# Optimization experiments

Hardware: AMD Instinct MI355X
Metric: run time of the kernel (lower is better)

The kernel has to match this reference:

```python
import jax, jax.numpy as jnp
import numpy as np
import math

LN_EPS = 1e-5


def setup_inputs() -> dict:
    key = jax.random.key(0)
    ks = jax.random.split(key, 6)
    B, S, D = 4, 4096, 1024
    x = jax.random.normal(ks[0], (B, S, D), dtype=jnp.float32)
    # torch.nn.Linear default init ~ U(-1/sqrt(fan_in), 1/sqrt(fan_in)); use scaled normal
    W_omega = jax.random.normal(ks[1], (D, D), dtype=jnp.float32) / math.sqrt(D)
    b_omega = jnp.zeros((D,), dtype=jnp.float32)
    log_scale = jnp.full((D,), math.log(0.1), dtype=jnp.float32)
    ln_gamma = jnp.ones((4 * D,), dtype=jnp.float32)
    ln_beta = jnp.zeros((4 * D,), dtype=jnp.float32)
    W1 = jax.random.normal(ks[2], (2 * D, 4 * D), dtype=jnp.float32) / math.sqrt(4 * D)
    b1 = jnp.zeros((2 * D,), dtype=jnp.float32)
    W2 = jax.random.normal(ks[3], (D, 2 * D), dtype=jnp.float32) / math.sqrt(2 * D)
    b2 = jnp.zeros((D,), dtype=jnp.float32)
    return {"x": x, "W_omega": W_omega, "b_omega": b_omega, "log_scale": log_scale,
            "ln_gamma": ln_gamma, "ln_beta": ln_beta, "W1": W1, "b1": b1, "W2": W2, "b2": b2}


def _layernorm(h, gamma, beta):
    mu = jnp.mean(h, axis=-1, keepdims=True)
    var = jnp.var(h, axis=-1, keepdims=True)
    return (h - mu) * jax.lax.rsqrt(var + LN_EPS) * gamma + beta


def reference(x, W_omega, b_omega, log_scale, ln_gamma, ln_beta, W1, b1, W2, b2):
    B, S, D = x.shape
    omega = jnp.einsum('bsd,ed->bse', x, W_omega) + b_omega  # Linear(dim, dim)
    position = jnp.arange(1, S + 1, dtype=x.dtype).reshape(1, S, 1)
    pos_scale = 1.0 / jnp.sqrt(position)
    omega_scaled = omega * jnp.exp(log_scale) * pos_scale
    phi = jnp.cumsum(omega_scaled, axis=1)
    cos_phi = jnp.cos(phi)
    sin_phi = jnp.sin(phi)
    cm_real = x * cos_phi  # content modulated (also cumsum input)
    cm_imag = x * sin_phi
    mem_real = jnp.cumsum(cm_real, axis=1) / position
    mem_imag = jnp.cumsum(cm_imag, axis=1) / position
    ret_real = mem_real * cos_phi + mem_imag * sin_phi
    ret_imag = mem_imag * cos_phi - mem_real * sin_phi
    context = jnp.concatenate([cm_real, cm_imag, ret_real, ret_imag], axis=-1)  # [B,S,4D]
    h = _layernorm(context, ln_gamma, ln_beta)
    h = jnp.einsum('bsd,ed->bse', h, W1) + b1
    h = jax.nn.gelu(h, approximate=False)  # torch nn.GELU default is exact erf form
    h = jnp.einsum('bsd,ed->bse', h, W2) + b2  # dropout is identity in eval mode
    return x + h
```

## Files before the change

kernel.cpp:

```cpp
#include <hip/hip_runtime.h>
#include <math.h>
#include <stddef.h>

#define BB 4
#define SS 4096
#define DD 1024

typedef unsigned short u16;
typedef __attribute__((ext_vector_type(4))) float f32x4;
typedef __attribute__((ext_vector_type(8))) short short8;
typedef __attribute__((ext_vector_type(4))) unsigned short u16x4;

#define EPI_BIAS  0
#define EPI_GELU  1
#define EPI_RESID 2

__device__ __forceinline__ u16 f2bf(float f) {
    unsigned u = __builtin_bit_cast(unsigned, f);
    u = (u + 0x7fffu + ((u >> 16) & 1u)) >> 16;
    return (u16)u;
}
__device__ __forceinline__ float bf2f(u16 h) {
    unsigned u = ((unsigned)h) << 16;
    return __builtin_bit_cast(float, u);
}

__device__ __forceinline__ void gll16(const void* g, void* l) {
    __builtin_amdgcn_global_load_lds(
        (const __attribute__((address_space(1))) void*)g,
        (__attribute__((address_space(3))) void*)l, 16, 0, 0);
}

template <int EPI>
__global__ __launch_bounds__(256) void gemm_bf(
    const u16* __restrict__ A, const u16* __restrict__ B,
    const float* __restrict__ bias, const float* __restrict__ resid,
    void* __restrict__ Cout, int M, int N, int K)
{
    __shared__ __align__(16) u16 Asm[128 * 64];
    __shared__ __align__(16) u16 Bsm[128 * 64];

    const int t = threadIdx.x;
    const int lane = t & 63;
    const int wave = t >> 6;
    const int wr = wave >> 1, wc = wave & 1;
    const int l15 = lane & 15, l4 = lane >> 4;
    const int bm = blockIdx.y * 128, bn = blockIdx.x * 128;

    const int r8 = lane >> 3, ch = lane & 7;
    const int schunk = ((ch ^ r8) << 3);

    const unsigned rmask = (unsigned)((l15 & 7) << 4);
    unsigned aoff[4][2], boff[4][2];
#pragma unroll
    for (int m = 0; m < 4; ++m)
#pragma unroll
        for (int ks = 0; ks < 2; ++ks) {
            const unsigned kb = ((((unsigned)ks << 6) | ((unsigned)l4 << 4)) ^ rmask);
            aoff[m][ks] = (unsigned)((wr * 64 + m * 16 + l15) * 128) + kb;
            boff[m][ks] = (unsigned)((wc * 64 + m * 16 + l15) * 128) + kb;
        }

    f32x4 acc[4][4];
#pragma unroll
    for (int m = 0; m < 4; ++m)
#pragma unroll
        for (int n = 0; n < 4; ++n) acc[m][n] = (f32x4)0.f;

    const char* acb = (const char*)Asm;
    const char* bcb = (const char*)Bsm;

    for (int k0 = 0; k0 < K; k0 += 64) {
        __syncthreads();
#pragma unroll
        for (int j = 0; j < 4; ++j) {
            const int rr = (wave * 4 + j) * 8 + r8;
            gll16(A + (size_t)(bm + rr) * K + k0 + schunk, (void*)(Asm + (wave * 4 + j) * 512));
            gll16(B + (size_t)(bn + rr) * K + k0 + schunk, (void*)(Bsm + (wave * 4 + j) * 512));
        }
        __syncthreads();
#pragma unroll
        for (int ks = 0; ks < 2; ++ks) {
            short8 af[4], bfr[4];
#pragma unroll
            for (int m = 0; m < 4; ++m) af[m] = *(const short8*)(acb + aoff[m][ks]);
#pragma unroll
            for (int n = 0; n < 4; ++n) bfr[n] = *(const short8*)(bcb + boff[n][ks]);
#pragma unroll
            for (int n = 0; n < 4; ++n)
#pragma unroll
                for (int m = 0; m < 4; ++m)
                    acc[m][n] = __builtin_amdgcn_mfma_f32_16x16x32_bf16(
                        af[m], bfr[n], acc[m][n], 0, 0, 0);
        }
    }

#pragma unroll
    for (int n = 0; n < 4; ++n) {
        const int col = bn + wc * 64 + n * 16 + l15;
        const float bvn = bias[col];
#pragma unroll
        for (int m = 0; m < 4; ++m) {
            const int row0 = bm + wr * 64 + m * 16 + l4 * 4;
#pragma unroll
            for (int r = 0; r < 4; ++r) {
                float v = acc[m][n][r] + bvn;
                if (EPI == EPI_GELU) {
                    v = 0.5f * v * (1.0f + erff(v * 0.70710678118654752f));
                    ((u16*)Cout)[(size_t)(row0 + r) * N + col] = f2bf(v);
                } else if (EPI == EPI_RESID) {
                    v += resid[(size_t)(row0 + r) * N + col];
                    ((float*)Cout)[(size_t)(row0 + r) * N + col] = v;
                } else {
                    ((float*)Cout)[(size_t)(row0 + r) * N + col] = v;
                }
            }
        }
    }
}

__global__ __launch_bounds__(256) void conv_hi(
    const float* __restrict__ s, u16* __restrict__ d, int n4,
    float* __restrict__ zstats)
{
    if (zstats != nullptr && blockIdx.x == 0) {
        for (int i = threadIdx.x; i < SS * 2; i += 256) zstats[i] = 0.f;
    }
    const int stride = gridDim.x * 256;
    for (int i = blockIdx.x * 256 + threadIdx.x; i < n4; i += stride) {
        const float4 v = ((const float4*)s)[i];
        u16x4 o = {f2bf(v.x), f2bf(v.y), f2bf(v.z), f2bf(v.w)};
        ((u16x4*)d)[i] = o;
    }
}

__global__ __launch_bounds__(1024) void scan_kernel(
    const float* __restrict__ omega, const float* __restrict__ x,
    const float* __restrict__ log_scale, u16* __restrict__ ctxH,
    float* __restrict__ stats)
{
    __shared__ float p_phi[64][16];
    __shared__ float p_r[64][16];
    __shared__ float p_i[64][16];

    const int t = threadIdx.x;
    const int dsub = t & 15;
    const int chunk = t >> 4;
    const int d = blockIdx.x * 16 + dsub;

    const float esc = expf(log_scale[d]);
    const size_t base = (size_t)chunk * 64 * DD + d;
    const float* om = omega + base;
    const float* xp = x + base;
    u16* cb = ctxH + (size_t)chunk * 64 * 4096 + d;

    float run = 0.f;
#pragma unroll 4
    for (int i = 0; i < 64; ++i) {
        const int s = chunk * 64 + i;
        run += om[(size_t)i * DD] * esc * rsqrtf((float)(s + 1));
    }
    p_phi[chunk][dsub] = run;
    __syncthreads();
    if (t < 16) {
        float r2 = 0.f;
        for (int c = 0; c < 64; ++c) { const float v = p_phi[c][t]; p_phi[c][t] = r2; r2 += v; }
    }
    __syncthreads();
    const float phi0 = p_phi[chunk][dsub];

    float runp = phi0, rr = 0.f, ri = 0.f;
#pragma unroll 4
    for (int i = 0; i < 64; ++i) {
        const int s = chunk * 64 + i;
        runp += om[(size_t)i * DD] * esc * rsqrtf((float)(s + 1));
        float sn, cs;
        sincosf(runp, &sn, &cs);
        const float xr = xp[(size_t)i * DD];
        const float cr = xr * cs, ci = xr * sn;
        cb[(size_t)i * 4096]      = f2bf(cr);
        cb[(size_t)i * 4096 + DD] = f2bf(ci);
        rr += cr; ri += ci;
    }
    p_r[chunk][dsub] = rr;
    p_i[chunk][dsub] = ri;
    __syncthreads();
    if (t < 32) {
        const int dd = t & 15;
        float (*arr)[16] = (t < 16) ? p_r : p_i;
        float r2 = 0.f;
        for (int c = 0; c < 64; ++c) { const float v = arr[c][dd]; arr[c][dd] = r2; r2 += v; }
    }
    __syncthreads();
    const float r0 = p_r[chunk][dsub];
    const float i0 = p_i[chunk][dsub];

    runp = phi0; rr = r0; ri = i0;
#pragma unroll 2
    for (int i = 0; i < 64; ++i) {
        const int s = chunk * 64 + i;
        runp += om[(size_t)i * DD] * esc * rsqrtf((float)(s + 1));
        float sn, cs;
        sincosf(runp, &sn, &cs);
        const float xr = xp[(size_t)i * DD];
        const float cr = xr * cs, ci = xr * sn;
        rr += cr; ri += ci;
        const float inv = 1.0f / (float)(s + 1);
        const float mr = rr * inv, mi = ri * inv;
        const float rtr = mr * cs + mi * sn;
        const float rti = mi * cs - mr * sn;
        cb[(size_t)i * 4096 + 2 * DD] = f2bf(rtr);
        cb[(size_t)i * 4096 + 3 * DD] = f2bf(rti);
        float vs = cr + ci + rtr + rti;
        float vq = cr * cr + ci * ci + rtr * rtr + rti * rti;
#pragma unroll
        for (int o = 1; o < 16; o <<= 1) {
            vs += __shfl_xor(vs, o);
            vq += __shfl_xor(vq, o);
        }
        if (dsub == 0) {
            atomicAdd(&stats[2 * s], vs);
            atomicAdd(&stats[2 * s + 1], vq);
        }
    }
}

__global__ __launch_bounds__(256) void ln_norm(
    u16* __restrict__ ctx, const float* __restrict__ stats,
    const float* __restrict__ gamma, const float* __restrict__ beta)
{
    const int row = blockIdx.x;
    const float mean = stats[2 * row] * (1.f / 4096.f);
    const float var = stats[2 * row + 1] * (1.f / 4096.f) - mean * mean;
    const float rs = rsqrtf(var + 1e-5f);
    u16* rp = ctx + (size_t)row * 4096;
    const int t = threadIdx.x;
#pragma unroll
    for (int it = 0; it < 2; ++it) {
        const int c0 = (t + it * 256) * 8;
        short8 v = *(short8*)(rp + c0);
        const float4 g0 = ((const float4*)(gamma + c0))[0];
        const float4 g1 = ((const float4*)(gamma + c0))[1];
        const float4 b0 = ((const float4*)(beta + c0))[0];
        const float4 b1 = ((const float4*)(beta + c0))[1];
        const float gv[8] = {g0.x, g0.y, g0.z, g0.w, g1.x, g1.y, g1.z, g1.w};
        const float bv[8] = {b0.x, b0.y, b0.z, b0.w, b1.x, b1.y, b1.z, b1.w};
        short8 o;
#pragma unroll
        for (int j = 0; j < 8; ++j) {
            const float f = bf2f((u16)v[j]);
            o[j] = (short)f2bf((f - mean) * rs * gv[j] + bv[j]);
        }
        *(short8*)(rp + c0) = o;
    }
}

extern "C" void kernel_launch(void* const* d_in, const int* in_sizes, int n_in,
                              void* d_out, int out_size, void* d_ws, size_t ws_size,
                              hipStream_t stream)
{
    (void)in_sizes; (void)n_in; (void)out_size; (void)ws_size;
    const float* x         = (const float*)d_in[0];
    const float* W_omega   = (const float*)d_in[1];
    const float* b_omega   = (const float*)d_in[2];
    const float* log_scale = (const float*)d_in[3];
    const float* ln_gamma  = (const float*)d_in[4];
    const float* ln_beta   = (const float*)d_in[5];
    const float* W1        = (const float*)d_in[6];
    const float* b1        = (const float*)d_in[7];
    const float* W2        = (const float*)d_in[8];
    const float* b2        = (const float*)d_in[9];
    float* out = (float*)d_out;

    char* ws = (char*)d_ws;
    u16*   ctxH  = (u16*)ws;
    float* omega = (float*)(ws + (size_t)32 * 1024 * 1024);
    u16*   h1H   = (u16*)omega;
    u16*   xH    = (u16*)(ws + (size_t)48 * 1024 * 1024);
    u16*   WomH  = (u16*)(ws + (size_t)56 * 1024 * 1024);
    u16*   W1H   = (u16*)(ws + (size_t)58 * 1024 * 1024);
    u16*   W2H   = (u16*)(ws + (size_t)74 * 1024 * 1024);
    float* stats = (float*)(ws + (size_t)78 * 1024 * 1024);

    conv_hi<<<dim3(512),  dim3(256), 0, stream>>>(W_omega, WomH, (DD * DD) / 4, nullptr);
    conv_hi<<<dim3(2048), dim3(256), 0, stream>>>(W1, W1H, (2 * DD * 4 * DD) / 4, nullptr);
    conv_hi<<<dim3(1024), dim3(256), 0, stream>>>(W2, W2H, (DD * 2 * DD) / 4, nullptr);

    for (int b = 0; b < BB; ++b) {
        const float* x_b = x + (size_t)b * SS * DD;
        float* out_b = out + (size_t)b * SS * DD;

        conv_hi<<<dim3(2048), dim3(256), 0, stream>>>(x_b, xH, (SS * DD) / 4, stats);

        gemm_bf<EPI_BIAS><<<dim3(DD / 128, SS / 128), dim3(256), 0, stream>>>(
            xH, WomH, b_omega, nullptr, omega, SS, DD, DD);

        scan_kernel<<<dim3(DD / 16), dim3(1024), 0, stream>>>(
            omega, x_b, log_scale, ctxH, stats);

        ln_norm<<<dim3(SS), dim3(256), 0, stream>>>(ctxH, stats, ln_gamma, ln_beta);

        gemm_bf<EPI_GELU><<<dim3((2 * DD) / 128, SS / 128), dim3(256), 0, stream>>>(
            ctxH, W1H, b1, nullptr, h1H, SS, 2 * DD, 4 * DD);

        gemm_bf<EPI_RESID><<<dim3(DD / 128, SS / 128), dim3(256), 0, stream>>>(
            h1H, W2H, b2, x_b, out_b, SS, DD, 2 * DD);
    }
}
```

Baseline: 1.350 ms.

## Batch LayerNorm and FFN GEMMs across multiple batch elements when workspace allows

```diff
diff --git a/kernel.cpp b/kernel.cpp
--- a/kernel.cpp
+++ b/kernel.cpp
@@ -120,18 +120,20 @@
 }
 
 __global__ __launch_bounds__(256) void conv_hi(
-    const float* __restrict__ s, u16* __restrict__ d, int n4,
-    float* __restrict__ zstats)
-{
-    if (zstats != nullptr && blockIdx.x == 0) {
-        for (int i = threadIdx.x; i < SS * 2; i += 256) zstats[i] = 0.f;
-    }
+    const float* __restrict__ s, u16* __restrict__ d, int n4)
+{
     const int stride = gridDim.x * 256;
     for (int i = blockIdx.x * 256 + threadIdx.x; i < n4; i += stride) {
         const float4 v = ((const float4*)s)[i];
         u16x4 o = {f2bf(v.x), f2bf(v.y), f2bf(v.z), f2bf(v.w)};
         ((u16x4*)d)[i] = o;
     }
+}
+
+__global__ __launch_bounds__(256) void zero_f32(float* __restrict__ p, int n)
+{
+    const int stride = gridDim.x * 256;
+    for (int i = blockIdx.x * 256 + threadIdx.x; i < n; i += stride) p[i] = 0.f;
 }
 
 __global__ __launch_bounds__(1024) void scan_kernel(
@@ -259,7 +261,7 @@
                               void* d_out, int out_size, void* d_ws, size_t ws_size,
                               hipStream_t stream)
 {
-    (void)in_sizes; (void)n_in; (void)out_size; (void)ws_size;
+    (void)in_sizes; (void)n_in; (void)out_size;
     const float* x         = (const float*)d_in[0];
     const float* W_omega   = (const float*)d_in[1];
     const float* b_omega   = (const float*)d_in[2];
@@ -272,38 +274,52 @@
     const float* b2        = (const float*)d_in[9];
     float* out = (float*)d_out;
 
+    const size_t MB1 = 1024 * 1024;
+    int G = 1;
+    {
+        const size_t need4 = (size_t)(4 * 48 + 30 + 1) * MB1;
+        const size_t need2 = (size_t)(2 * 48 + 30 + 1) * MB1;
+        if (ws_size >= need4) G = 4;
+        else if (ws_size >= need2) G = 2;
+    }
+
     char* ws = (char*)d_ws;
     u16*   ctxH  = (u16*)ws;
-    float* omega = (float*)(ws + (size_t)32 * 1024 * 1024);
-    u16*   h1H   = (u16*)omega;
-    u16*   xH    = (u16*)(ws + (size_t)48 * 1024 * 1024);
-    u16*   WomH  = (u16*)(ws + (size_t)56 * 1024 * 1024);
-    u16*   W1H   = (u16*)(ws + (size_t)58 * 1024 * 1024);
-    u16*   W2H   = (u16*)(ws + (size_t)74 * 1024 * 1024);
-    float* stats = (float*)(ws + (size_t)78 * 1024 * 1024);
-
-    conv_hi<<<dim3(512),  dim3(256), 0, stream>>>(W_omega, WomH, (DD * DD) / 4, nullptr);
-    conv_hi<<<dim3(2048), dim3(256), 0, stream>>>(W1, W1H, (2 * DD * 4 * DD) / 4, nullptr);
-    conv_hi<<<dim3(1024), dim3(256), 0, stream>>>(W2, W2H, (DD * 2 * DD) / 4, nullptr);
-
-    for (int b = 0; b < BB; ++b) {
-        const float* x_b = x + (size_t)b * SS * DD;
-        float* out_b = out + (size_t)b * SS * DD;
-
-        conv_hi<<<dim3(2048), dim3(256), 0, stream>>>(x_b, xH, (SS * DD) / 4, stats);
-
-        gemm_bf<EPI_BIAS><<<dim3(DD / 128, SS / 128), dim3(256), 0, stream>>>(
-            xH, WomH, b_omega, nullptr, omega, SS, DD, DD);
-
-        scan_kernel<<<dim3(DD / 16), dim3(1024), 0, stream>>>(
-            omega, x_b, log_scale, ctxH, stats);
-
-        ln_norm<<<dim3(SS), dim3(256), 0, stream>>>(ctxH, stats, ln_gamma, ln_beta);
-
-        gemm_bf<EPI_GELU><<<dim3((2 * DD) / 128, SS / 128), dim3(256), 0, stream>>>(
-            ctxH, W1H, b1, nullptr, h1H, SS, 2 * DD, 4 * DD);
-
-        gemm_bf<EPI_RESID><<<dim3(DD / 128, SS / 128), dim3(256), 0, stream>>>(
-            h1H, W2H, b2, x_b, out_b, SS, DD, 2 * DD);
-    }
-}
+    u16*   h1H   = (u16*)(ws + (size_t)G * 32 * MB1);
+    float* omega = (float*)h1H;
+    u16*   xHb   = (u16*)(ws + (size_t)G * 48 * MB1);
+    u16*   WomH  = (u16*)(ws + (size_t)G * 48 * MB1 + 8 * MB1);
+    u16*   W1H   = (u16*)(ws + (size_t)G * 48 * MB1 + 10 * MB1);
+    u16*   W2H   = (u16*)(ws + (size_t)G * 48 * MB1 + 26 * MB1);
+    float* stats = (float*)(ws + (size_t)G * 48 * MB1 + 30 * MB1);
+
+    conv_hi<<<dim3(512),  dim3(256), 0, stream>>>(W_omega, WomH, (DD * DD) / 4);
+    conv_hi<<<dim3(2048), dim3(256), 0, stream>>>(W1, W1H, (2 * DD * 4 * DD) / 4);
+    conv_hi<<<dim3(1024), dim3(256), 0, stream>>>(W2, W2H, (DD * 2 * DD) / 4);
+
+    for (int g0 = 0; g0 < BB; g0 += G) {
+        const int Mg = G * SS;
+        zero_f32<<<dim3(32), dim3(256), 0, stream>>>(stats, Mg * 2);
+
+        for (int bi = 0; bi < G; ++bi) {
+            const int b = g0 + bi;
+            const float* x_b = x + (size_t)b * SS * DD;
+
+            conv_hi<<<dim3(2048), dim3(256), 0, stream>>>(x_b, xHb, (SS * DD) / 4);
+            gemm_bf<EPI_BIAS><<<dim3(DD / 128, SS / 128), dim3(256), 0, stream>>>(
+                xHb, WomH, b_omega, nullptr, omega, SS, DD, DD);
+            scan_kernel<<<dim3(DD / 16), dim3(1024), 0, stream>>>(
+                omega, x_b, log_scale,
+                ctxH + (size_t)bi * SS * 4096, stats + (size_t)bi * SS * 2);
+        }
+
+        ln_norm<<<dim3(Mg), dim3(256), 0, stream>>>(ctxH, stats, ln_gamma, ln_beta);
+
+        gemm_bf<EPI_GELU><<<dim3((2 * DD) / 128, Mg / 128), dim3(256), 0, stream>>>(
+            ctxH, W1H, b1, nullptr, h1H, Mg, 2 * DD, 4 * DD);
+
+        gemm_bf<EPI_RESID><<<dim3(DD / 128, Mg / 128), dim3(256), 0, stream>>>(
+            h1H, W2H, b2, x + (size_t)g0 * SS * DD, out + (size_t)g0 * SS * DD,
+            Mg, DD, 2 * DD);
+    }
+}
```

Result: faster. 1.284 ms (-4.9%).
